# Kernel tuning notes

Hardware: AMD Instinct MI355X
Metric: run time of the kernel (lower is better)

The kernel has to match this reference:

```python
import jax, jax.numpy as jnp
import numpy as np

B, T, D = 1, 4096, 1024
H, KD, VD = 16, 64, 64
MIN_THETA, MAX_THETA = 1.0, 10000.0


def setup_inputs() -> dict:
    key = jax.random.key(0)
    k0, k1, k2 = jax.random.split(key, 3)
    x = jax.random.normal(k0, (B, T, D), dtype=jnp.float32)
    W_in = jax.random.normal(k1, ((2 * KD + VD) * H, D), dtype=jnp.float32) * 0.02
    b_in = jnp.zeros(((2 * KD + VD) * H,), dtype=jnp.float32)
    W_out = jax.random.normal(k2, (D, H * VD), dtype=jnp.float32) * 0.02
    b_out = jnp.zeros((D,), dtype=jnp.float32)
    return {"x": x, "W_in": W_in, "b_in": b_in, "W_out": W_out, "b_out": b_out}


def _sin_cos(t, d, dtype):
    # geometric sequence of thetas over half the head dim
    half = d // 2
    p = jnp.arange(half, dtype=dtype) / (half - 1)
    thetas = MIN_THETA * (MAX_THETA / MIN_THETA) ** p  # [half]
    pos = jnp.arange(t, dtype=dtype)[:, None] / thetas[None, :]  # [T, half]
    return jnp.sin(pos), jnp.cos(pos)


def _rope(x, sin, cos):
    d = x.shape[-1] // 2
    x_hi, x_lo = x[..., :d], x[..., d:]
    y_lo = x_lo * cos + x_hi * sin
    y_hi = x_hi * cos - x_lo * sin
    return jnp.concatenate([y_lo, y_hi], axis=-1)


def reference(x, W_in, b_in, W_out, b_out):
    b, t, _ = x.shape
    proj = x @ W_in.T + b_in  # [B, T, (2KD+VD)*H]
    i1, i2 = KD * H, 2 * KD * H
    q = proj[..., :i1].reshape(b, t, H, KD).transpose(0, 2, 1, 3)   # [B,H,T,KD]
    k = proj[..., i1:i2].reshape(b, t, H, KD).transpose(0, 2, 1, 3)
    v = proj[..., i2:].reshape(b, t, H, VD).transpose(0, 2, 1, 3)   # [B,H,T,VD]
    sin, cos = _sin_cos(t, KD, x.dtype)
    q = _rope(q, sin, cos)
    k = _rope(k, sin, cos)
    scale = 1.0 / np.sqrt(KD)
    att = jnp.einsum('bhqd,bhkd->bhqk', q, k) * jnp.asarray(scale, x.dtype)
    mask = jnp.tril(jnp.ones((t, t), dtype=bool))  # causal
    att = jnp.where(mask[None, None], att, jnp.asarray(-jnp.inf, x.dtype))
    att = jax.nn.softmax(att, axis=-1)
    y = jnp.einsum('bhqk,bhkd->bhqd', att, v)
    y = y.transpose(0, 2, 1, 3).reshape(b, t, H * VD)
    return y @ W_out.T + b_out
```

## Files before the change

### kernel.cpp

```cpp
#include <hip/hip_runtime.h>
#include <math.h>

#define T_SEQ 4096
#define DMODEL 1024
#define NH 16
#define HD 64
#define NQT (T_SEQ / 64)

typedef _Float16 f16x4 __attribute__((ext_vector_type(4)));
typedef _Float16 f16x8 __attribute__((ext_vector_type(8)));
typedef float f32x4 __attribute__((ext_vector_type(4)));

#define HTD ((size_t)NH * T_SEQ * HD)

__global__ __launch_bounds__(256)
void sincos_table_kernel(float* __restrict__ tab) {
    int idx = blockIdx.x * 256 + threadIdx.x;
    if (idx >= T_SEQ * 32) return;
    int t = idx >> 5, j = idx & 31;
    double p = (double)((float)j / 31.0f);
    float theta = (float)pow(10000.0, p);
    float ang = (float)t / theta;
    double a = (double)ang;
    tab[t * 64 + j]      = (float)sin(a);
    tab[t * 64 + 32 + j] = (float)cos(a);
}

__global__ __launch_bounds__(256)
void cast3_kernel(const float* __restrict__ x, const float* __restrict__ wi,
                  const float* __restrict__ wo, _Float16* __restrict__ x16,
                  _Float16* __restrict__ wi16, _Float16* __restrict__ wo16) {
    size_t gid = (size_t)blockIdx.x * 256 + threadIdx.x;
    const float* src; _Float16* dst; size_t i;
    if (gid < 524288)       { src = x;  dst = x16;  i = gid; }
    else if (gid < 917504)  { src = wi; dst = wi16; i = gid - 524288; }
    else                    { src = wo; dst = wo16; i = gid - 917504; }
    float4 a = *((const float4*)src + i * 2);
    float4 b = *((const float4*)src + i * 2 + 1);
    f16x8 o = {(_Float16)a.x, (_Float16)a.y, (_Float16)a.z, (_Float16)a.w,
               (_Float16)b.x, (_Float16)b.y, (_Float16)b.z, (_Float16)b.w};
    *((f16x8*)dst + i) = o;
}

__global__ __launch_bounds__(256)
void rope_kernel(float* __restrict__ q, const float* __restrict__ k,
                 _Float16* __restrict__ k16, const float* __restrict__ tab) {
    int idx = blockIdx.x * 256 + threadIdx.x;
    int j = idx & 31;
    int t = (idx >> 5) & (T_SEQ - 1);
    int h = (idx >> 17) & (NH - 1);
    int z = idx >> 21;
    float s = tab[t * 64 + j];
    float c = tab[t * 64 + 32 + j];
    size_t off = ((size_t)h * T_SEQ + t) * HD;
    if (z == 0) {
        float* base = q + off;
        float a = base[j], b = base[j + 32];
        base[j]      = b * c + a * s;
        base[j + 32] = a * c - b * s;
    } else {
        const float* base = k + off;
        float a = base[j], b = base[j + 32];
        k16[off + j]      = (_Float16)(b * c + a * s);
        k16[off + j + 32] = (_Float16)(a * c - b * s);
    }
}

template<int EPI>
__global__ __launch_bounds__(256)
void gemm16_kernel(const _Float16* __restrict__ A, const _Float16* __restrict__ B,
                   const float* __restrict__ bias, float* __restrict__ out,
                   _Float16* __restrict__ outv, int M, int N, int K, int gx) {
    __shared__ _Float16 Alds[128 * 64];
    __shared__ _Float16 Blds[128 * 64];
    const int tid = threadIdx.x;
    const int w = tid >> 6, lane = tid & 63, lq = lane & 15, lg = lane >> 4;
    const int wr = w >> 1, wc = w & 1;

    int cpx = (int)gridDim.x >> 3;
    int tileid = (blockIdx.x & 7) * cpx + (blockIdx.x >> 3);
    const int bx = tileid % gx, by = tileid / gx;
    const int row0 = by * 128, col0 = bx * 128;

    const int ra = tid >> 1, ha = tid & 1;
    const _Float16* Ap = A + (size_t)(row0 + ra) * K + ha * 32;
    const _Float16* Bp = B + (size_t)(col0 + ra) * K + ha * 32;
    char* Awr = (char*)Alds + ra * 128;
    char* Bwr = (char*)Blds + ra * 128;
    int wsw[4];
#pragma unroll
    for (int j = 0; j < 4; ++j) wsw[j] = ((ha * 4 + j) ^ (ra & 7)) * 16;

    f32x4 acc[4][4] = {};
    f16x8 sa[4], sb[4];
#pragma unroll
    for (int j = 0; j < 4; ++j) {
        sa[j] = *(const f16x8*)(Ap + j * 8);
        sb[j] = *(const f16x8*)(Bp + j * 8);
    }

    const int nkt = K >> 6;
    for (int kt = 0; kt < nkt; ++kt) {
        __syncthreads();
#pragma unroll
        for (int j = 0; j < 4; ++j) {
            *(f16x8*)(Awr + wsw[j]) = sa[j];
            *(f16x8*)(Bwr + wsw[j]) = sb[j];
        }
        __syncthreads();
        if (kt + 1 < nkt) {
            int kn = (kt + 1) << 6;
#pragma unroll
            for (int j = 0; j < 4; ++j) {
                sa[j] = *(const f16x8*)(Ap + kn + j * 8);
                sb[j] = *(const f16x8*)(Bp + kn + j * 8);
            }
        }
#pragma unroll
        for (int ks = 0; ks < 2; ++ks) {
            f16x8 af[4], bf[4];
            const int cofs = ((ks * 4 + lg) ^ (lq & 7)) * 16;
#pragma unroll
            for (int i = 0; i < 4; ++i) {
                int rA = wr * 64 + i * 16 + lq;
                int rB = wc * 64 + i * 16 + lq;
                af[i] = *(const f16x8*)((char*)Alds + rA * 128 + cofs);
                bf[i] = *(const f16x8*)((char*)Blds + rB * 128 + cofs);
            }
#pragma unroll
            for (int mi = 0; mi < 4; ++mi)
#pragma unroll
                for (int nj = 0; nj < 4; ++nj)
                    acc[mi][nj] = __builtin_amdgcn_mfma_f32_16x16x32_f16(
                        af[mi], bf[nj], acc[mi][nj], 0, 0, 0);
        }
    }

    if (EPI == 0) {
#pragma unroll
        for (int nj = 0; nj < 4; ++nj) {
            int n = col0 + wc * 64 + nj * 16 + lq;
            float bv = bias[n];
#pragma unroll
            for (int mi = 0; mi < 4; ++mi) {
                int t0 = row0 + wr * 64 + mi * 16 + lg * 4;
#pragma unroll
                for (int r = 0; r < 4; ++r)
                    out[(size_t)(t0 + r) * N + n] = acc[mi][nj][r] + bv;
            }
        }
    } else {
        const int tensor = col0 >> 10;
        const int m0b = row0 + wr * 64;
        if (tensor == 2) {
#pragma unroll
            for (int nj = 0; nj < 4; ++nj) {
                int n = col0 + wc * 64 + nj * 16 + lq;
                int nn = n & 1023; int hh = nn >> 6, d = nn & 63;
                float bv = bias[n];
                _Float16* dv = outv + (size_t)(hh * 64 + d) * T_SEQ;
#pragma unroll
                for (int mi = 0; mi < 4; ++mi) {
                    int t0 = m0b + mi * 16 + lg * 4;
                    f16x4 val = {(_Float16)(acc[mi][nj][0] + bv),
                                 (_Float16)(acc[mi][nj][1] + bv),
                                 (_Float16)(acc[mi][nj][2] + bv),
                                 (_Float16)(acc[mi][nj][3] + bv)};
                    *(f16x4*)(dv + t0) = val;
                }
            }
        } else {
            float* dst = out + (size_t)tensor * HTD;
#pragma unroll
            for (int nj = 0; nj < 4; ++nj) {
                int n = col0 + wc * 64 + nj * 16 + lq;
                int nn = n & 1023; int hh = nn >> 6, d = nn & 63;
                float bv = bias[n];
                float* dcol = dst + (size_t)hh * T_SEQ * HD + d;
#pragma unroll
                for (int mi = 0; mi < 4; ++mi) {
                    int t0 = m0b + mi * 16 + lg * 4;
#pragma unroll
                    for (int r = 0; r < 4; ++r)
                        dcol[(size_t)(t0 + r) * HD] = acc[mi][nj][r] + bv;
                }
            }
        }
    }
}

__global__ __launch_bounds__(256)
void attn_kernel(const float* __restrict__ qb, const _Float16* __restrict__ k16,
                 const _Float16* __restrict__ v16t, _Float16* __restrict__ y16) {
    __shared__ _Float16 Klds[64 * 64];
    __shared__ _Float16 Vlds[64 * 64];
    __shared__ _Float16 Plds[4 * 16 * 64];

    const int tid  = threadIdx.x;
    const int w    = tid >> 6;
    const int lane = tid & 63;
    const int lq   = lane & 15;
    const int lg   = lane >> 4;

    const int bid = blockIdx.x;
    const int h   = ((bid & 7) << 1) | ((bid >> 3) & 1);
    const int qt  = (NQT - 1) - (bid >> 4);
    const int q0  = qt * 64;

    const float*    qh = qb   + (size_t)h * T_SEQ * HD;
    const _Float16* kh = k16  + (size_t)h * T_SEQ * HD;
    const _Float16* vh = v16t + (size_t)h * HD * T_SEQ;

    const int qrow = q0 + w * 16 + lq;
    f16x8 qf[2];
#pragma unroll
    for (int ks = 0; ks < 2; ++ks) {
        float4 a = *(const float4*)(qh + (size_t)qrow * HD + lg * 8 + ks * 32);
        float4 b = *(const float4*)(qh + (size_t)qrow * HD + lg * 8 + ks * 32 + 4);
        f16x8 t = {(_Float16)(a.x * 0.125f), (_Float16)(a.y * 0.125f),
                   (_Float16)(a.z * 0.125f), (_Float16)(a.w * 0.125f),
                   (_Float16)(b.x * 0.125f), (_Float16)(b.y * 0.125f),
                   (_Float16)(b.z * 0.125f), (_Float16)(b.w * 0.125f)};
        qf[ks] = t;
    }

    const int srow = tid >> 4;
    const int scol = (tid & 15) * 4;
    const int schk = (tid & 15) >> 1;
    const int ssub = (tid & 1) * 8;

    float m_r = -3e38f, l_r = 0.f;
    f32x4 acco[4] = {};

    _Float16* Pw = Plds + w * 1024;

    for (int kt = 0; kt <= qt; ++kt) {
        const int k0 = kt * 64;
        f16x4 kreg[4], vreg[4];
#pragma unroll
        for (int it = 0; it < 4; ++it) {
            int row = srow + it * 16;
            kreg[it] = *(const f16x4*)(kh + (size_t)(k0 + row) * HD + scol);
            vreg[it] = *(const f16x4*)(vh + (size_t)row * T_SEQ + k0 + scol);
        }
        __syncthreads();
#pragma unroll
        for (int it = 0; it < 4; ++it) {
            int row = srow + it * 16;
            int chunk = schk ^ (row & 7);
            *(f16x4*)((char*)Klds + row * 128 + chunk * 16 + ssub) = kreg[it];
            *(f16x4*)((char*)Vlds + row * 128 + chunk * 16 + ssub) = vreg[it];
        }
        __syncthreads();

        f32x4 s[4] = {};
#pragma unroll
        for (int mb = 0; mb < 4; ++mb) {
            int row = mb * 16 + lq;
#pragma unroll
            for (int ks = 0; ks < 2; ++ks) {
                f16x8 kf = *(const f16x8*)((char*)Klds + row * 128 +
                                           (((lg + 4 * ks) ^ (lq & 7)) * 16));
                s[mb] = __builtin_amdgcn_mfma_f32_16x16x32_f16(kf, qf[ks], s[mb], 0, 0, 0);
            }
        }
        if (kt == qt) {
            const int qloc = w * 16 + lq;
#pragma unroll
            for (int mb = 0; mb < 4; ++mb)
#pragma unroll
                for (int r = 0; r < 4; ++r)
                    if (mb * 16 + lg * 4 + r > qloc) s[mb][r] = -3e38f;
        }

        float tmax = s[0][0];
#pragma unroll
        for (int mb = 0; mb < 4; ++mb)
#pragma unroll
            for (int r = 0; r < 4; ++r) tmax = fmaxf(tmax, s[mb][r]);
        tmax = fmaxf(tmax, __shfl_xor(tmax, 16));
        tmax = fmaxf(tmax, __shfl_xor(tmax, 32));
        float mn  = fmaxf(m_r, tmax);
        float scl = __expf(m_r - mn);
        m_r = mn;

        float tsum = 0.f;
#pragma unroll
        for (int mb = 0; mb < 4; ++mb) {
            float p0 = __expf(s[mb][0] - mn), p1 = __expf(s[mb][1] - mn);
            float p2 = __expf(s[mb][2] - mn), p3 = __expf(s[mb][3] - mn);
            tsum += (p0 + p1) + (p2 + p3);
            f16x4 pk = {(_Float16)p0, (_Float16)p1, (_Float16)p2, (_Float16)p3};
            *(f16x4*)(Pw + (mb * 2 + (lg >> 1)) * 128 + lq * 8 + (lg & 1) * 4) = pk;
        }
        tsum += __shfl_xor(tsum, 16);
        tsum += __shfl_xor(tsum, 32);
        l_r = l_r * scl + tsum;
#pragma unroll
        for (int mb = 0; mb < 4; ++mb)
#pragma unroll
            for (int r = 0; r < 4; ++r) acco[mb][r] *= scl;

        f16x8 pf[2];
#pragma unroll
        for (int ks = 0; ks < 2; ++ks)
            pf[ks] = *(const f16x8*)(Pw + (lg + 4 * ks) * 128 + lq * 8);
#pragma unroll
        for (int mb = 0; mb < 4; ++mb) {
            int row = mb * 16 + lq;
#pragma unroll
            for (int ks = 0; ks < 2; ++ks) {
                f16x8 vf = *(const f16x8*)((char*)Vlds + row * 128 +
                                           (((lg + 4 * ks) ^ (lq & 7)) * 16));
                acco[mb] = __builtin_amdgcn_mfma_f32_16x16x32_f16(vf, pf[ks], acco[mb], 0, 0, 0);
            }
        }
    }

    float inv = 1.f / l_r;
#pragma unroll
    for (int mb = 0; mb < 4; ++mb) {
        f16x4 o = {(_Float16)(acco[mb][0] * inv), (_Float16)(acco[mb][1] * inv),
                   (_Float16)(acco[mb][2] * inv), (_Float16)(acco[mb][3] * inv)};
        *(f16x4*)(y16 + (size_t)qrow * DMODEL + h * HD + mb * 16 + lg * 4) = o;
    }
}

extern "C" void kernel_launch(void* const* d_in, const int* in_sizes, int n_in,
                              void* d_out, int out_size, void* d_ws, size_t ws_size,
                              hipStream_t stream) {
    const float* x     = (const float*)d_in[0];
    const float* W_in  = (const float*)d_in[1];
    const float* b_in  = (const float*)d_in[2];
    const float* W_out = (const float*)d_in[3];
    const float* b_out = (const float*)d_in[4];
    float* out = (float*)d_out;

    float* ws = (float*)d_ws;
    float* q_ws = ws;
    float* k_ws = ws + HTD;
    float* tab  = ws + 2 * HTD;
    _Float16* f16b = (_Float16*)(ws + 2 * HTD + (size_t)T_SEQ * 64);
    _Float16* k16  = f16b;
    _Float16* v16t = k16 + HTD;
    _Float16* x16  = v16t + HTD;
    _Float16* y16  = x16;
    _Float16* wi16 = x16 + (size_t)T_SEQ * DMODEL;
    _Float16* wo16 = wi16 + (size_t)3072 * DMODEL;

    sincos_table_kernel<<<(T_SEQ * 32 + 255) / 256, 256, 0, stream>>>(tab);
    cast3_kernel<<<4096, 256, 0, stream>>>(x, W_in, W_out, x16, wi16, wo16);

    gemm16_kernel<1><<<768, 256, 0, stream>>>(
        x16, wi16, b_in, q_ws, v16t, T_SEQ, 3072, DMODEL, 24);

    rope_kernel<<<(2 * NH * T_SEQ * 32) / 256, 256, 0, stream>>>(q_ws, k_ws, k16, tab);

    attn_kernel<<<NQT * NH, 256, 0, stream>>>(q_ws, k16, v16t, y16);

    gemm16_kernel<0><<<256, 256, 0, stream>>>(
        y16, wo16, b_out, out, nullptr, T_SEQ, DMODEL, DMODEL, 8);
}
```

Baseline: 238.9 us.

## Store Q/K in fp16, double-buffer attention tiles, pair causal query tiles per block

```diff
diff --git a/kernel.cpp b/kernel.cpp
--- a/kernel.cpp
+++ b/kernel.cpp
@@ -43,8 +43,8 @@
 }
 
 __global__ __launch_bounds__(256)
-void rope_kernel(float* __restrict__ q, const float* __restrict__ k,
-                 _Float16* __restrict__ k16, const float* __restrict__ tab) {
+void rope16_kernel(_Float16* __restrict__ q16, _Float16* __restrict__ k16,
+                   const float* __restrict__ tab) {
     int idx = blockIdx.x * 256 + threadIdx.x;
     int j = idx & 31;
     int t = (idx >> 5) & (T_SEQ - 1);
@@ -52,18 +52,13 @@
     int z = idx >> 21;
     float s = tab[t * 64 + j];
     float c = tab[t * 64 + 32 + j];
-    size_t off = ((size_t)h * T_SEQ + t) * HD;
-    if (z == 0) {
-        float* base = q + off;
-        float a = base[j], b = base[j + 32];
-        base[j]      = b * c + a * s;
-        base[j + 32] = a * c - b * s;
-    } else {
-        const float* base = k + off;
-        float a = base[j], b = base[j + 32];
-        k16[off + j]      = (_Float16)(b * c + a * s);
-        k16[off + j + 32] = (_Float16)(a * c - b * s);
-    }
+    _Float16* base = (z ? k16 : q16) + ((size_t)h * T_SEQ + t) * HD;
+    float a = (float)base[j], b = (float)base[j + 32];
+    float lo = b * c + a * s;
+    float hi = a * c - b * s;
+    if (z == 0) { lo *= 0.125f; hi *= 0.125f; }
+    base[j]      = (_Float16)lo;
+    base[j + 32] = (_Float16)hi;
 }
 
 template<int EPI>
@@ -158,7 +153,7 @@
                 int n = col0 + wc * 64 + nj * 16 + lq;
                 int nn = n & 1023; int hh = nn >> 6, d = nn & 63;
                 float bv = bias[n];
-                _Float16* dv = outv + (size_t)(hh * 64 + d) * T_SEQ;
+                _Float16* dv = outv + 2 * HTD + (size_t)(hh * 64 + d) * T_SEQ;
 #pragma unroll
                 for (int mi = 0; mi < 4; ++mi) {
                     int t0 = m0b + mi * 16 + lg * 4;
@@ -170,19 +165,19 @@
                 }
             }
         } else {
-            float* dst = out + (size_t)tensor * HTD;
+            _Float16* dst = outv + (size_t)tensor * HTD;
 #pragma unroll
             for (int nj = 0; nj < 4; ++nj) {
                 int n = col0 + wc * 64 + nj * 16 + lq;
                 int nn = n & 1023; int hh = nn >> 6, d = nn & 63;
                 float bv = bias[n];
-                float* dcol = dst + (size_t)hh * T_SEQ * HD + d;
+                _Float16* dcol = dst + (size_t)hh * T_SEQ * HD + d;
 #pragma unroll
                 for (int mi = 0; mi < 4; ++mi) {
                     int t0 = m0b + mi * 16 + lg * 4;
 #pragma unroll
                     for (int r = 0; r < 4; ++r)
-                        dcol[(size_t)(t0 + r) * HD] = acc[mi][nj][r] + bv;
+                        dcol[(size_t)(t0 + r) * HD] = (_Float16)(acc[mi][nj][r] + bv);
                 }
             }
         }
@@ -190,10 +185,10 @@
 }
 
 __global__ __launch_bounds__(256)
-void attn_kernel(const float* __restrict__ qb, const _Float16* __restrict__ k16,
+void attn_kernel(const _Float16* __restrict__ q16, const _Float16* __restrict__ k16,
                  const _Float16* __restrict__ v16t, _Float16* __restrict__ y16) {
-    __shared__ _Float16 Klds[64 * 64];
-    __shared__ _Float16 Vlds[64 * 64];
+    __shared__ _Float16 Klds[2][64 * 64];
+    __shared__ _Float16 Vlds[2][64 * 64];
     __shared__ _Float16 Plds[4 * 16 * 64];
 
     const int tid  = threadIdx.x;
@@ -202,127 +197,151 @@
     const int lq   = lane & 15;
     const int lg   = lane >> 4;
 
-    const int bid = blockIdx.x;
-    const int h   = ((bid & 7) << 1) | ((bid >> 3) & 1);
-    const int qt  = (NQT - 1) - (bid >> 4);
-    const int q0  = qt * 64;
-
-    const float*    qh = qb   + (size_t)h * T_SEQ * HD;
+    const int bid  = blockIdx.x;
+    const int h    = ((bid & 7) << 1) | ((bid >> 3) & 1);
+    const int pr   = bid >> 4;
+
+    const _Float16* qh = q16  + (size_t)h * T_SEQ * HD;
     const _Float16* kh = k16  + (size_t)h * T_SEQ * HD;
     const _Float16* vh = v16t + (size_t)h * HD * T_SEQ;
-
-    const int qrow = q0 + w * 16 + lq;
-    f16x8 qf[2];
-#pragma unroll
-    for (int ks = 0; ks < 2; ++ks) {
-        float4 a = *(const float4*)(qh + (size_t)qrow * HD + lg * 8 + ks * 32);
-        float4 b = *(const float4*)(qh + (size_t)qrow * HD + lg * 8 + ks * 32 + 4);
-        f16x8 t = {(_Float16)(a.x * 0.125f), (_Float16)(a.y * 0.125f),
-                   (_Float16)(a.z * 0.125f), (_Float16)(a.w * 0.125f),
-                   (_Float16)(b.x * 0.125f), (_Float16)(b.y * 0.125f),
-                   (_Float16)(b.z * 0.125f), (_Float16)(b.w * 0.125f)};
-        qf[ks] = t;
-    }
 
     const int srow = tid >> 4;
     const int scol = (tid & 15) * 4;
     const int schk = (tid & 15) >> 1;
     const int ssub = (tid & 1) * 8;
 
-    float m_r = -3e38f, l_r = 0.f;
-    f32x4 acco[4] = {};
-
     _Float16* Pw = Plds + w * 1024;
 
-    for (int kt = 0; kt <= qt; ++kt) {
-        const int k0 = kt * 64;
+    for (int half = 0; half < 2; ++half) {
+        const int qt = half ? pr : (NQT - 1 - pr);
+        const int q0 = qt * 64;
+        const int qrow = q0 + w * 16 + lq;
+
+        f16x8 qf[2];
+        qf[0] = *(const f16x8*)(qh + (size_t)qrow * HD + lg * 8);
+        qf[1] = *(const f16x8*)(qh + (size_t)qrow * HD + lg * 8 + 32);
+
+        float m_r = -3e38f, l_r = 0.f;
+        f32x4 acco[4] = {};
+
         f16x4 kreg[4], vreg[4];
 #pragma unroll
         for (int it = 0; it < 4; ++it) {
             int row = srow + it * 16;
-            kreg[it] = *(const f16x4*)(kh + (size_t)(k0 + row) * HD + scol);
-            vreg[it] = *(const f16x4*)(vh + (size_t)row * T_SEQ + k0 + scol);
+            kreg[it] = *(const f16x4*)(kh + (size_t)row * HD + scol);
+            vreg[it] = *(const f16x4*)(vh + (size_t)row * T_SEQ + scol);
         }
         __syncthreads();
 #pragma unroll
         for (int it = 0; it < 4; ++it) {
             int row = srow + it * 16;
             int chunk = schk ^ (row & 7);
-            *(f16x4*)((char*)Klds + row * 128 + chunk * 16 + ssub) = kreg[it];
-            *(f16x4*)((char*)Vlds + row * 128 + chunk * 16 + ssub) = vreg[it];
-        }
-        __syncthreads();
-
-        f32x4 s[4] = {};
+            *(f16x4*)((char*)Klds[0] + row * 128 + chunk * 16 + ssub) = kreg[it];
+            *(f16x4*)((char*)Vlds[0] + row * 128 + chunk * 16 + ssub) = vreg[it];
+        }
+
+        int cur = 0;
+        for (int kt = 0; kt <= qt; ++kt) {
+            __syncthreads();
+            if (kt < qt) {
+                const int k0n = (kt + 1) * 64;
+#pragma unroll
+                for (int it = 0; it < 4; ++it) {
+                    int row = srow + it * 16;
+                    kreg[it] = *(const f16x4*)(kh + (size_t)(k0n + row) * HD + scol);
+                    vreg[it] = *(const f16x4*)(vh + (size_t)row * T_SEQ + k0n + scol);
+                }
+            }
+
+            f32x4 s[4] = {};
+            __builtin_amdgcn_s_setprio(1);
+#pragma unroll
+            for (int mb = 0; mb < 4; ++mb) {
+                int row = mb * 16 + lq;
+#pragma unroll
+                for (int ks = 0; ks < 2; ++ks) {
+                    f16x8 kf = *(const f16x8*)((char*)Klds[cur] + row * 128 +
+                                               (((lg + 4 * ks) ^ (lq & 7)) * 16));
+                    s[mb] = __builtin_amdgcn_mfma_f32_16x16x32_f16(kf, qf[ks], s[mb], 0, 0, 0);
+                }
+            }
+            __builtin_amdgcn_s_setprio(0);
+            if (kt == qt) {
+                const int qloc = w * 16 + lq;
+#pragma unroll
+                for (int mb = 0; mb < 4; ++mb)
+#pragma unroll
+                    for (int r = 0; r < 4; ++r)
+                        if (mb * 16 + lg * 4 + r > qloc) s[mb][r] = -3e38f;
+            }
+
+            float tmax = s[0][0];
+#pragma unroll
+            for (int mb = 0; mb < 4; ++mb)
+#pragma unroll
+                for (int r = 0; r < 4; ++r) tmax = fmaxf(tmax, s[mb][r]);
+            tmax = fmaxf(tmax, __shfl_xor(tmax, 16));
+            tmax = fmaxf(tmax, __shfl_xor(tmax, 32));
+            if (__ballot(tmax > m_r + 8.0f)) {
+                float mn  = fmaxf(m_r, tmax);
+                float scl = __expf(m_r - mn);
+                m_r = mn;
+                l_r *= scl;
+#pragma unroll
+                for (int mb = 0; mb < 4; ++mb)
+#pragma unroll
+                    for (int r = 0; r < 4; ++r) acco[mb][r] *= scl;
+            }
+
+            float tsum = 0.f;
+#pragma unroll
+            for (int mb = 0; mb < 4; ++mb) {
+                float p0 = __expf(s[mb][0] - m_r), p1 = __expf(s[mb][1] - m_r);
+                float p2 = __expf(s[mb][2] - m_r), p3 = __expf(s[mb][3] - m_r);
+                tsum += (p0 + p1) + (p2 + p3);
+                f16x4 pk = {(_Float16)p0, (_Float16)p1, (_Float16)p2, (_Float16)p3};
+                *(f16x4*)(Pw + (mb * 2 + (lg >> 1)) * 128 + lq * 8 + (lg & 1) * 4) = pk;
+            }
+            tsum += __shfl_xor(tsum, 16);
+            tsum += __shfl_xor(tsum, 32);
+            l_r += tsum;
+
+            f16x8 pf[2];
+#pragma unroll
+            for (int ks = 0; ks < 2; ++ks)
+                pf[ks] = *(const f16x8*)(Pw + (lg + 4 * ks) * 128 + lq * 8);
+            __builtin_amdgcn_s_setprio(1);
+#pragma unroll
+            for (int mb = 0; mb < 4; ++mb) {
+                int row = mb * 16 + lq;
+#pragma unroll
+                for (int ks = 0; ks < 2; ++ks) {
+                    f16x8 vf = *(const f16x8*)((char*)Vlds[cur] + row * 128 +
+                                               (((lg + 4 * ks) ^ (lq & 7)) * 16));
+                    acco[mb] = __builtin_amdgcn_mfma_f32_16x16x32_f16(vf, pf[ks], acco[mb], 0, 0, 0);
+                }
+            }
+            __builtin_amdgcn_s_setprio(0);
+
+            if (kt < qt) {
+#pragma unroll
+                for (int it = 0; it < 4; ++it) {
+                    int row = srow + it * 16;
+                    int chunk = schk ^ (row & 7);
+                    *(f16x4*)((char*)Klds[cur ^ 1] + row * 128 + chunk * 16 + ssub) = kreg[it];
+                    *(f16x4*)((char*)Vlds[cur ^ 1] + row * 128 + chunk * 16 + ssub) = vreg[it];
+                }
+                cur ^= 1;
+            }
+        }
+
+        float inv = 1.f / l_r;
 #pragma unroll
         for (int mb = 0; mb < 4; ++mb) {
-            int row = mb * 16 + lq;
-#pragma unroll
-            for (int ks = 0; ks < 2; ++ks) {
-                f16x8 kf = *(const f16x8*)((char*)Klds + row * 128 +
-                                           (((lg + 4 * ks) ^ (lq & 7)) * 16));
-                s[mb] = __builtin_amdgcn_mfma_f32_16x16x32_f16(kf, qf[ks], s[mb], 0, 0, 0);
-            }
-        }
-        if (kt == qt) {
-            const int qloc = w * 16 + lq;
-#pragma unroll
-            for (int mb = 0; mb < 4; ++mb)
-#pragma unroll
-                for (int r = 0; r < 4; ++r)
-                    if (mb * 16 + lg * 4 + r > qloc) s[mb][r] = -3e38f;
-        }
-
-        float tmax = s[0][0];
-#pragma unroll
-        for (int mb = 0; mb < 4; ++mb)
-#pragma unroll
-            for (int r = 0; r < 4; ++r) tmax = fmaxf(tmax, s[mb][r]);
-        tmax = fmaxf(tmax, __shfl_xor(tmax, 16));
-        tmax = fmaxf(tmax, __shfl_xor(tmax, 32));
-        float mn  = fmaxf(m_r, tmax);
-        float scl = __expf(m_r - mn);
-        m_r = mn;
-
-        float tsum = 0.f;
-#pragma unroll
-        for (int mb = 0; mb < 4; ++mb) {
-            float p0 = __expf(s[mb][0] - mn), p1 = __expf(s[mb][1] - mn);
-            float p2 = __expf(s[mb][2] - mn), p3 = __expf(s[mb][3] - mn);
-            tsum += (p0 + p1) + (p2 + p3);
-            f16x4 pk = {(_Float16)p0, (_Float16)p1, (_Float16)p2, (_Float16)p3};
-            *(f16x4*)(Pw + (mb * 2 + (lg >> 1)) * 128 + lq * 8 + (lg & 1) * 4) = pk;
-        }
-        tsum += __shfl_xor(tsum, 16);
-        tsum += __shfl_xor(tsum, 32);
-        l_r = l_r * scl + tsum;
-#pragma unroll
-        for (int mb = 0; mb < 4; ++mb)
-#pragma unroll
-            for (int r = 0; r < 4; ++r) acco[mb][r] *= scl;
-
-        f16x8 pf[2];
-#pragma unroll
-        for (int ks = 0; ks < 2; ++ks)
-            pf[ks] = *(const f16x8*)(Pw + (lg + 4 * ks) * 128 + lq * 8);
-#pragma unroll
-        for (int mb = 0; mb < 4; ++mb) {
-            int row = mb * 16 + lq;
-#pragma unroll
-            for (int ks = 0; ks < 2; ++ks) {
-                f16x8 vf = *(const f16x8*)((char*)Vlds + row * 128 +
-                                           (((lg + 4 * ks) ^ (lq & 7)) * 16));
-                acco[mb] = __builtin_amdgcn_mfma_f32_16x16x32_f16(vf, pf[ks], acco[mb], 0, 0, 0);
-            }
-        }
-    }
-
-    float inv = 1.f / l_r;
-#pragma unroll
-    for (int mb = 0; mb < 4; ++mb) {
-        f16x4 o = {(_Float16)(acco[mb][0] * inv), (_Float16)(acco[mb][1] * inv),
-                   (_Float16)(acco[mb][2] * inv), (_Float16)(acco[mb][3] * inv)};
-        *(f16x4*)(y16 + (size_t)qrow * DMODEL + h * HD + mb * 16 + lg * 4) = o;
+            f16x4 o = {(_Float16)(acco[mb][0] * inv), (_Float16)(acco[mb][1] * inv),
+                       (_Float16)(acco[mb][2] * inv), (_Float16)(acco[mb][3] * inv)};
+            *(f16x4*)(y16 + (size_t)qrow * DMODEL + h * HD + mb * 16 + lg * 4) = o;
+        }
     }
 }
 
@@ -337,13 +356,12 @@
     float* out = (float*)d_out;
 
     float* ws = (float*)d_ws;
-    float* q_ws = ws;
-    float* k_ws = ws + HTD;
-    float* tab  = ws + 2 * HTD;
-    _Float16* f16b = (_Float16*)(ws + 2 * HTD + (size_t)T_SEQ * 64);
-    _Float16* k16  = f16b;
-    _Float16* v16t = k16 + HTD;
-    _Float16* x16  = v16t + HTD;
+    float* tab = ws;
+    _Float16* fb   = (_Float16*)(ws + (size_t)T_SEQ * 64);
+    _Float16* q16  = fb;
+    _Float16* k16  = fb + HTD;
+    _Float16* v16t = fb + 2 * HTD;
+    _Float16* x16  = fb + 3 * HTD;
     _Float16* y16  = x16;
     _Float16* wi16 = x16 + (size_t)T_SEQ * DMODEL;
     _Float16* wo16 = wi16 + (size_t)3072 * DMODEL;
@@ -352,11 +370,11 @@
     cast3_kernel<<<4096, 256, 0, stream>>>(x, W_in, W_out, x16, wi16, wo16);
 
     gemm16_kernel<1><<<768, 256, 0, stream>>>(
-        x16, wi16, b_in, q_ws, v16t, T_SEQ, 3072, DMODEL, 24);
-
-    rope_kernel<<<(2 * NH * T_SEQ * 32) / 256, 256, 0, stream>>>(q_ws, k_ws, k16, tab);
-
-    attn_kernel<<<NQT * NH, 256, 0, stream>>>(q_ws, k16, v16t, y16);
+        x16, wi16, b_in, nullptr, q16, T_SEQ, 3072, DMODEL, 24);
+
+    rope16_kernel<<<(2 * NH * T_SEQ * 32) / 256, 256, 0, stream>>>(q16, k16, tab);
+
+    attn_kernel<<<512, 256, 0, stream>>>(q16, k16, v16t, y16);
 
     gemm16_kernel<0><<<256, 256, 0, stream>>>(
         y16, wo16, b_out, out, nullptr, T_SEQ, DMODEL, DMODEL, 8);
```

After: 237.1 us. No clear change (-0.8%).
